# Kernel optimization log

Measured on AMD Instinct MI355X. Metric: run time of the kernel, lower is better.

## Reference

```python
import math
import jax, jax.numpy as jnp
import numpy as np

B, CK, H, W = 4, 64, 48, 84


def setup_inputs() -> dict:
    key = jax.random.key(0)
    k1, k2 = jax.random.split(key)
    mk = jax.random.normal(k1, (B, CK, 1, H, W), dtype=jnp.float32)
    qk = jax.random.normal(k2, (B, CK, H, W), dtype=jnp.float32)
    return {"mk": mk, "qk": qk}


def reference(mk, qk):
    b_, ck = mk.shape[0], mk.shape[1]
    mkf = mk.reshape(b_, ck, -1)            # [B, CK, N]  (N = T*H*W, T=1)
    qkf = qk.reshape(b_, ck, -1)            # [B, CK, M]  (M = H*W)
    a = jnp.sum(mkf * mkf, axis=1)[:, :, None]              # [B, N, 1]
    b = 2.0 * jnp.einsum('bcn,bcm->bnm', mkf, qkf)          # [B, N, M]
    c = jnp.sum(qkf * qkf, axis=1)[:, None, :]              # [B, 1, M]
    affinity = (-a + b - c) / math.sqrt(ck)                 # -||mk - qk||^2 / sqrt(CK)
    return jax.nn.softmax(affinity, axis=1)                 # softmax over memory axis
```

## Files before the change

kernel.cpp:

```cpp
#include <hip/hip_runtime.h>
#include <math.h>

#define B_  4
#define CK_ 64
#define N_  4032
#define M_  4032

#define P1_CHUNKS 7
#define P1_TILES  9
#define P2_GROUPS 9
#define P2_TILES  7

typedef __attribute__((ext_vector_type(8))) short short8;
typedef __attribute__((ext_vector_type(4))) float float4v;

__device__ inline unsigned short f2bf(float x) {
    unsigned u = __float_as_uint(x);
    u += 0x7FFF + ((u >> 16) & 1);
    return (unsigned short)(u >> 16);
}
__device__ inline float bf2f(unsigned short h) {
    return __uint_as_float(((unsigned)h) << 16);
}

__global__ __launch_bounds__(256) void prep_kernel(
    const float* __restrict__ mk, const float* __restrict__ qk,
    unsigned short* __restrict__ mk_hi, unsigned short* __restrict__ mk_lo,
    unsigned short* __restrict__ qk_hi, unsigned short* __restrict__ qk_lo,
    float* __restrict__ u)
{
    __shared__ float tile[64][65];
    __shared__ float sred[4][64];
    const int t  = threadIdx.x;
    const int n0 = blockIdx.x * 64;
    const int b  = blockIdx.y;
    const int which = blockIdx.z;

    const float* src = (which == 0 ? mk : qk) + (size_t)b * CK_ * N_;
    unsigned short* dhi = (which == 0 ? mk_hi : qk_hi) + (size_t)b * N_ * CK_;
    unsigned short* dlo = (which == 0 ? mk_lo : qk_lo) + (size_t)b * N_ * CK_;

    #pragma unroll
    for (int i = 0; i < 16; ++i) {
        const int idx = t + 256 * i;
        const int c = idx >> 6, n = idx & 63;
        tile[c][n] = src[(size_t)c * N_ + n0 + n];
    }
    __syncthreads();

    const int n = t & 63;
    const int g = t >> 6;
    unsigned short hbits[16], lbits[16];
    float ssq = 0.f;
    #pragma unroll
    for (int i = 0; i < 16; ++i) {
        const float x = tile[g * 16 + i][n];
        const unsigned short h = f2bf(x);
        hbits[i] = h;
        lbits[i] = f2bf(x - bf2f(h));
        ssq = fmaf(x, x, ssq);
    }
    {
        union { short8 v; unsigned short s[8]; } p0, p1, q0, q1;
        #pragma unroll
        for (int i = 0; i < 8; ++i) {
            p0.s[i] = hbits[i]; p1.s[i] = hbits[8 + i];
            q0.s[i] = lbits[i]; q1.s[i] = lbits[8 + i];
        }
        const size_t base = (size_t)(n0 + n) * CK_ + g * 16;
        *(short8*)(dhi + base)     = p0.v;
        *(short8*)(dhi + base + 8) = p1.v;
        *(short8*)(dlo + base)     = q0.v;
        *(short8*)(dlo + base + 8) = q1.v;
    }
    sred[g][n] = ssq;
    __syncthreads();
    if (which == 0 && t < 64) {
        const float tot = sred[0][t] + sred[1][t] + sred[2][t] + sred[3][t];
        u[(size_t)b * N_ + n0 + t] = __expf(-0.125f * tot);
    }
}


__global__ __launch_bounds__(256) void pass1_kernel(
    const unsigned short* __restrict__ mk_hi, const unsigned short* __restrict__ mk_lo,
    const unsigned short* __restrict__ qk_hi, const unsigned short* __restrict__ qk_lo,
    const float* __restrict__ u, float* __restrict__ psum)
{
    __shared__ float cs[2][64];
    const int t = threadIdx.x;
    const int wave = t >> 6, lane = t & 63;
    const int wn = wave & 1, wm = wave >> 1;
    const int lcol = lane & 15;
    const int quad = lane >> 4;
    const int chunk = blockIdx.y;
    const int b = blockIdx.z;
    const int m_base = blockIdx.x * 64 + wm * 32;

    const unsigned short* mh = mk_hi + (size_t)b * N_ * CK_;
    const unsigned short* ml = mk_lo + (size_t)b * N_ * CK_;
    const unsigned short* qh = qk_hi + (size_t)b * M_ * CK_;
    const unsigned short* ql = qk_lo + (size_t)b * M_ * CK_;
    const float* ub = u + (size_t)b * N_;

    short8 bh[2][2], bl[2][2];
    #pragma unroll
    for (int cg = 0; cg < 2; ++cg) {
        const size_t mrow = (size_t)(m_base + cg * 16 + lcol) * CK_;
        #pragma unroll
        for (int kc = 0; kc < 2; ++kc) {
            const size_t off = mrow + kc * 32 + quad * 8;
            bh[cg][kc] = *(const short8*)(qh + off);
            bl[cg][kc] = *(const short8*)(ql + off);
        }
    }

    float p0 = 0.f, p1 = 0.f;

    #pragma unroll 1
    for (int it = chunk * P1_TILES; it < chunk * P1_TILES + P1_TILES; ++it) {
        const int n_base = it * 64 + wn * 32;
        short8 ah[2][2], al[2][2];
        #pragma unroll
        for (int rg = 0; rg < 2; ++rg) {
            const size_t nrow = (size_t)(n_base + rg * 16 + lcol) * CK_;
            #pragma unroll
            for (int kc = 0; kc < 2; ++kc) {
                const size_t off = nrow + kc * 32 + quad * 8;
                ah[rg][kc] = *(const short8*)(mh + off);
                al[rg][kc] = *(const short8*)(ml + off);
            }
        }
        float uv[2][4];
        #pragma unroll
        for (int rg = 0; rg < 2; ++rg)
            #pragma unroll
            for (int r = 0; r < 4; ++r)
                uv[rg][r] = ub[n_base + rg * 16 + quad * 4 + r];

        #pragma unroll
        for (int rg = 0; rg < 2; ++rg) {
            #pragma unroll
            for (int cg = 0; cg < 2; ++cg) {
                float4v a1 = {0.f, 0.f, 0.f, 0.f};
                float4v a2 = {0.f, 0.f, 0.f, 0.f};
                #pragma unroll
                for (int kc = 0; kc < 2; ++kc) {
                    a1 = __builtin_amdgcn_mfma_f32_16x16x32_bf16(ah[rg][kc], bh[cg][kc], a1, 0, 0, 0);
                    a2 = __builtin_amdgcn_mfma_f32_16x16x32_bf16(ah[rg][kc], bl[cg][kc], a2, 0, 0, 0);
                    a2 = __builtin_amdgcn_mfma_f32_16x16x32_bf16(al[rg][kc], bh[cg][kc], a2, 0, 0, 0);
                }
                float ps = 0.f;
                #pragma unroll
                for (int r = 0; r < 4; ++r) {
                    const float dot = a1[r] + a2[r];
                    ps += uv[rg][r] * __expf(0.25f * dot);
                }
                if (cg == 0) p0 += ps; else p1 += ps;
            }
        }
    }

    p0 += __shfl_xor(p0, 16); p0 += __shfl_xor(p0, 32);
    p1 += __shfl_xor(p1, 16); p1 += __shfl_xor(p1, 32);
    if (lane < 16) {
        cs[wn][wm * 32 + lcol]      = p0;
        cs[wn][wm * 32 + 16 + lcol] = p1;
    }
    __syncthreads();
    if (t < 64) {
        psum[((size_t)b * P1_CHUNKS + chunk) * M_ + blockIdx.x * 64 + t] =
            cs[0][t] + cs[1][t];
    }
}

__global__ __launch_bounds__(256) void pass2_kernel(
    const unsigned short* __restrict__ mk_hi, const unsigned short* __restrict__ mk_lo,
    const unsigned short* __restrict__ qk_hi, const unsigned short* __restrict__ qk_lo,
    const float* __restrict__ u, const float* __restrict__ psum,
    float* __restrict__ out)
{
    const int t = threadIdx.x;
    const int wave = t >> 6, lane = t & 63;
    const int wn = wave & 1, wm = wave >> 1;
    const int lcol = lane & 15;
    const int quad = lane >> 4;
    const int b = blockIdx.z;
    const int m_base = blockIdx.x * 64 + wm * 32;

    const unsigned short* mh = mk_hi + (size_t)b * N_ * CK_;
    const unsigned short* ml = mk_lo + (size_t)b * N_ * CK_;
    const unsigned short* qh = qk_hi + (size_t)b * M_ * CK_;
    const unsigned short* ql = qk_lo + (size_t)b * M_ * CK_;
    const float* ub = u + (size_t)b * N_;

    short8 qah[2][2], qal[2][2];
    #pragma unroll
    for (int mg = 0; mg < 2; ++mg) {
        const size_t mrow = (size_t)(m_base + mg * 16 + lcol) * CK_;
        #pragma unroll
        for (int kc = 0; kc < 2; ++kc) {
            const size_t off = mrow + kc * 32 + quad * 8;
            qah[mg][kc] = *(const short8*)(qh + off);
            qal[mg][kc] = *(const short8*)(ql + off);
        }
    }

    float4v rinv4[2];
    #pragma unroll
    for (int mg = 0; mg < 2; ++mg) {
        float4v tot = {0.f, 0.f, 0.f, 0.f};
        #pragma unroll
        for (int c = 0; c < P1_CHUNKS; ++c) {
            const float4v p = *(const float4v*)(
                psum + ((size_t)b * P1_CHUNKS + c) * M_ + m_base + mg * 16 + quad * 4);
            tot += p;
        }
        rinv4[mg][0] = 1.f / tot[0];
        rinv4[mg][1] = 1.f / tot[1];
        rinv4[mg][2] = 1.f / tot[2];
        rinv4[mg][3] = 1.f / tot[3];
    }

    float* obase = out + (size_t)b * N_ * M_ + m_base + quad * 4;

    #pragma unroll 1
    for (int j = 0; j < P2_TILES; ++j) {
        const int n_base = (blockIdx.y * P2_TILES + j) * 64 + wn * 32;

        short8 bh[2][2], bl[2][2];
        #pragma unroll
        for (int ng = 0; ng < 2; ++ng) {
            const size_t nrow = (size_t)(n_base + ng * 16 + lcol) * CK_;
            #pragma unroll
            for (int kc = 0; kc < 2; ++kc) {
                const size_t off = nrow + kc * 32 + quad * 8;
                bh[ng][kc] = *(const short8*)(mh + off);
                bl[ng][kc] = *(const short8*)(ml + off);
            }
        }
        float un[2];
        #pragma unroll
        for (int ng = 0; ng < 2; ++ng)
            un[ng] = ub[n_base + ng * 16 + lcol];

        #pragma unroll
        for (int mg = 0; mg < 2; ++mg) {
            #pragma unroll
            for (int ng = 0; ng < 2; ++ng) {
                float4v a1 = {0.f, 0.f, 0.f, 0.f};
                float4v a2 = {0.f, 0.f, 0.f, 0.f};
                #pragma unroll
                for (int kc = 0; kc < 2; ++kc) {
                    a1 = __builtin_amdgcn_mfma_f32_16x16x32_bf16(qah[mg][kc], bh[ng][kc], a1, 0, 0, 0);
                    a2 = __builtin_amdgcn_mfma_f32_16x16x32_bf16(qah[mg][kc], bl[ng][kc], a2, 0, 0, 0);
                    a2 = __builtin_amdgcn_mfma_f32_16x16x32_bf16(qal[mg][kc], bh[ng][kc], a2, 0, 0, 0);
                }
                float4v v;
                #pragma unroll
                for (int r = 0; r < 4; ++r) {
                    const float dot = a1[r] + a2[r];
                    v[r] = un[ng] * __expf(0.25f * dot) * rinv4[mg][r];
                }
                float4v* dst = (float4v*)(
                    obase + (size_t)(n_base + ng * 16 + lcol) * M_ + mg * 16);
                __builtin_nontemporal_store(v, dst);
            }
        }
    }
}

extern "C" void kernel_launch(void* const* d_in, const int* in_sizes, int n_in,
                              void* d_out, int out_size, void* d_ws, size_t ws_size,
                              hipStream_t stream) {
    const float* mk = (const float*)d_in[0];
    const float* qk = (const float*)d_in[1];
    float* out = (float*)d_out;

    unsigned short* mk_hi = (unsigned short*)d_ws;
    unsigned short* mk_lo = mk_hi + (size_t)B_ * N_ * CK_;
    unsigned short* qk_hi = mk_lo + (size_t)B_ * N_ * CK_;
    unsigned short* qk_lo = qk_hi + (size_t)B_ * M_ * CK_;
    float* u    = (float*)(qk_lo + (size_t)B_ * M_ * CK_);
    float* psum = u + (size_t)B_ * N_;

    prep_kernel<<<dim3(N_ / 64, B_, 2), 256, 0, stream>>>(mk, qk, mk_hi, mk_lo, qk_hi, qk_lo, u);
    pass1_kernel<<<dim3(M_ / 64, P1_CHUNKS, B_), 256, 0, stream>>>(mk_hi, mk_lo, qk_hi, qk_lo, u, psum);
    pass2_kernel<<<dim3(M_ / 64, P2_GROUPS, B_), 256, 0, stream>>>(mk_hi, mk_lo, qk_hi, qk_lo, u, psum, out);
}
```

Before: 380.4 us.

## Pad N/M to 4096, use 512-thread blocks, unroll loops and raise MFMA priority

Pads the memory and query dimensions to 4096 with zeroed entries (u=0 for padded rows), so tile counts become powers of two. Blocks grow to 8 waves covering 128 query columns, main loops unroll by two, MFMA sections are wrapped in s_setprio, and the u values load as float4 vectors. The aim is better scheduling and latency hiding, with a guarded store that skips padded output. The cost is about 3% extra compute on padded rows plus a few branch checks.

```diff
diff --git a/kernel.cpp b/kernel.cpp
--- a/kernel.cpp
+++ b/kernel.cpp
@@ -5,11 +5,13 @@
 #define CK_ 64
 #define N_  4032
 #define M_  4032
-
-#define P1_CHUNKS 7
-#define P1_TILES  9
-#define P2_GROUPS 9
-#define P2_TILES  7
+#define NP_ 4096
+#define MP_ 4096
+
+#define P1C 8
+#define P1T 8
+#define P2G 8
+#define P2T 8
 
 typedef __attribute__((ext_vector_type(8))) short short8;
 typedef __attribute__((ext_vector_type(4))) float float4v;
@@ -35,16 +37,25 @@
     const int n0 = blockIdx.x * 64;
     const int b  = blockIdx.y;
     const int which = blockIdx.z;
+    const bool pad = (n0 >= N_);
 
     const float* src = (which == 0 ? mk : qk) + (size_t)b * CK_ * N_;
-    unsigned short* dhi = (which == 0 ? mk_hi : qk_hi) + (size_t)b * N_ * CK_;
-    unsigned short* dlo = (which == 0 ? mk_lo : qk_lo) + (size_t)b * N_ * CK_;
-
-    #pragma unroll
-    for (int i = 0; i < 16; ++i) {
-        const int idx = t + 256 * i;
-        const int c = idx >> 6, n = idx & 63;
-        tile[c][n] = src[(size_t)c * N_ + n0 + n];
+    unsigned short* dhi = (which == 0 ? mk_hi : qk_hi) + (size_t)b * NP_ * CK_;
+    unsigned short* dlo = (which == 0 ? mk_lo : qk_lo) + (size_t)b * NP_ * CK_;
+
+    if (!pad) {
+        #pragma unroll
+        for (int i = 0; i < 16; ++i) {
+            const int idx = t + 256 * i;
+            const int c = idx >> 6, n = idx & 63;
+            tile[c][n] = src[(size_t)c * N_ + n0 + n];
+        }
+    } else {
+        #pragma unroll
+        for (int i = 0; i < 16; ++i) {
+            const int idx = t + 256 * i;
+            tile[idx >> 6][idx & 63] = 0.f;
+        }
     }
     __syncthreads();
 
@@ -77,17 +88,17 @@
     __syncthreads();
     if (which == 0 && t < 64) {
         const float tot = sred[0][t] + sred[1][t] + sred[2][t] + sred[3][t];
-        u[(size_t)b * N_ + n0 + t] = __expf(-0.125f * tot);
-    }
-}
-
-
-__global__ __launch_bounds__(256) void pass1_kernel(
+        u[(size_t)b * NP_ + n0 + t] = pad ? 0.f : __expf(-0.125f * tot);
+    }
+}
+
+
+__global__ __launch_bounds__(512) void pass1_kernel(
     const unsigned short* __restrict__ mk_hi, const unsigned short* __restrict__ mk_lo,
     const unsigned short* __restrict__ qk_hi, const unsigned short* __restrict__ qk_lo,
     const float* __restrict__ u, float* __restrict__ psum)
 {
-    __shared__ float cs[2][64];
+    __shared__ float cs[2][128];
     const int t = threadIdx.x;
     const int wave = t >> 6, lane = t & 63;
     const int wn = wave & 1, wm = wave >> 1;
@@ -95,13 +106,13 @@
     const int quad = lane >> 4;
     const int chunk = blockIdx.y;
     const int b = blockIdx.z;
-    const int m_base = blockIdx.x * 64 + wm * 32;
-
-    const unsigned short* mh = mk_hi + (size_t)b * N_ * CK_;
-    const unsigned short* ml = mk_lo + (size_t)b * N_ * CK_;
-    const unsigned short* qh = qk_hi + (size_t)b * M_ * CK_;
-    const unsigned short* ql = qk_lo + (size_t)b * M_ * CK_;
-    const float* ub = u + (size_t)b * N_;
+    const int m_base = blockIdx.x * 128 + wm * 32;
+
+    const unsigned short* mh = mk_hi + (size_t)b * NP_ * CK_;
+    const unsigned short* ml = mk_lo + (size_t)b * NP_ * CK_;
+    const unsigned short* qh = qk_hi + (size_t)b * NP_ * CK_;
+    const unsigned short* ql = qk_lo + (size_t)b * NP_ * CK_;
+    const float* ub = u + (size_t)b * NP_;
 
     short8 bh[2][2], bl[2][2];
     #pragma unroll
@@ -117,8 +128,8 @@
 
     float p0 = 0.f, p1 = 0.f;
 
-    #pragma unroll 1
-    for (int it = chunk * P1_TILES; it < chunk * P1_TILES + P1_TILES; ++it) {
+    #pragma unroll 2
+    for (int it = chunk * P1T; it < chunk * P1T + P1T; ++it) {
         const int n_base = it * 64 + wn * 32;
         short8 ah[2][2], al[2][2];
         #pragma unroll
@@ -131,12 +142,8 @@
                 al[rg][kc] = *(const short8*)(ml + off);
             }
         }
-        float uv[2][4];
-        #pragma unroll
-        for (int rg = 0; rg < 2; ++rg)
-            #pragma unroll
-            for (int r = 0; r < 4; ++r)
-                uv[rg][r] = ub[n_base + rg * 16 + quad * 4 + r];
+        float4v uv0 = *(const float4v*)(ub + n_base + quad * 4);
+        float4v uv1 = *(const float4v*)(ub + n_base + 16 + quad * 4);
 
         #pragma unroll
         for (int rg = 0; rg < 2; ++rg) {
@@ -144,17 +151,20 @@
             for (int cg = 0; cg < 2; ++cg) {
                 float4v a1 = {0.f, 0.f, 0.f, 0.f};
                 float4v a2 = {0.f, 0.f, 0.f, 0.f};
+                __builtin_amdgcn_s_setprio(1);
                 #pragma unroll
                 for (int kc = 0; kc < 2; ++kc) {
                     a1 = __builtin_amdgcn_mfma_f32_16x16x32_bf16(ah[rg][kc], bh[cg][kc], a1, 0, 0, 0);
                     a2 = __builtin_amdgcn_mfma_f32_16x16x32_bf16(ah[rg][kc], bl[cg][kc], a2, 0, 0, 0);
                     a2 = __builtin_amdgcn_mfma_f32_16x16x32_bf16(al[rg][kc], bh[cg][kc], a2, 0, 0, 0);
                 }
+                __builtin_amdgcn_s_setprio(0);
                 float ps = 0.f;
                 #pragma unroll
                 for (int r = 0; r < 4; ++r) {
                     const float dot = a1[r] + a2[r];
-                    ps += uv[rg][r] * __expf(0.25f * dot);
+                    const float uvr = (rg == 0) ? uv0[r] : uv1[r];
+                    ps += uvr * __expf(0.25f * dot);
                 }
                 if (cg == 0) p0 += ps; else p1 += ps;
             }
@@ -168,13 +178,13 @@
         cs[wn][wm * 32 + 16 + lcol] = p1;
     }
     __syncthreads();
-    if (t < 64) {
-        psum[((size_t)b * P1_CHUNKS + chunk) * M_ + blockIdx.x * 64 + t] =
+    if (t < 128) {
+        psum[((size_t)b * P1C + chunk) * MP_ + blockIdx.x * 128 + t] =
             cs[0][t] + cs[1][t];
     }
 }
 
-__global__ __launch_bounds__(256) void pass2_kernel(
+__global__ __launch_bounds__(512) void pass2_kernel(
     const unsigned short* __restrict__ mk_hi, const unsigned short* __restrict__ mk_lo,
     const unsigned short* __restrict__ qk_hi, const unsigned short* __restrict__ qk_lo,
     const float* __restrict__ u, const float* __restrict__ psum,
@@ -186,13 +196,13 @@
     const int lcol = lane & 15;
     const int quad = lane >> 4;
     const int b = blockIdx.z;
-    const int m_base = blockIdx.x * 64 + wm * 32;
-
-    const unsigned short* mh = mk_hi + (size_t)b * N_ * CK_;
-    const unsigned short* ml = mk_lo + (size_t)b * N_ * CK_;
-    const unsigned short* qh = qk_hi + (size_t)b * M_ * CK_;
-    const unsigned short* ql = qk_lo + (size_t)b * M_ * CK_;
-    const float* ub = u + (size_t)b * N_;
+    const int m_base = blockIdx.x * 128 + wm * 32;
+
+    const unsigned short* mh = mk_hi + (size_t)b * NP_ * CK_;
+    const unsigned short* ml = mk_lo + (size_t)b * NP_ * CK_;
+    const unsigned short* qh = qk_hi + (size_t)b * NP_ * CK_;
+    const unsigned short* ql = qk_lo + (size_t)b * NP_ * CK_;
+    const float* ub = u + (size_t)b * NP_;
 
     short8 qah[2][2], qal[2][2];
     #pragma unroll
@@ -211,9 +221,9 @@
     for (int mg = 0; mg < 2; ++mg) {
         float4v tot = {0.f, 0.f, 0.f, 0.f};
         #pragma unroll
-        for (int c = 0; c < P1_CHUNKS; ++c) {
+        for (int c = 0; c < P1C; ++c) {
             const float4v p = *(const float4v*)(
-                psum + ((size_t)b * P1_CHUNKS + c) * M_ + m_base + mg * 16 + quad * 4);
+                psum + ((size_t)b * P1C + c) * MP_ + m_base + mg * 16 + quad * 4);
             tot += p;
         }
         rinv4[mg][0] = 1.f / tot[0];
@@ -222,11 +232,14 @@
         rinv4[mg][3] = 1.f / tot[3];
     }
 
+    const bool mval0 = (m_base < N_);
+    const bool mval1 = (m_base + 16 < N_);
+
     float* obase = out + (size_t)b * N_ * M_ + m_base + quad * 4;
 
-    #pragma unroll 1
-    for (int j = 0; j < P2_TILES; ++j) {
-        const int n_base = (blockIdx.y * P2_TILES + j) * 64 + wn * 32;
+    #pragma unroll 2
+    for (int j = 0; j < P2T; ++j) {
+        const int n_base = (blockIdx.y * P2T + j) * 64 + wn * 32;
 
         short8 bh[2][2], bl[2][2];
         #pragma unroll
@@ -244,27 +257,33 @@
         for (int ng = 0; ng < 2; ++ng)
             un[ng] = ub[n_base + ng * 16 + lcol];
 
+        const bool nval = (n_base < N_);
+
         #pragma unroll
         for (int mg = 0; mg < 2; ++mg) {
             #pragma unroll
             for (int ng = 0; ng < 2; ++ng) {
                 float4v a1 = {0.f, 0.f, 0.f, 0.f};
                 float4v a2 = {0.f, 0.f, 0.f, 0.f};
+                __builtin_amdgcn_s_setprio(1);
                 #pragma unroll
                 for (int kc = 0; kc < 2; ++kc) {
                     a1 = __builtin_amdgcn_mfma_f32_16x16x32_bf16(qah[mg][kc], bh[ng][kc], a1, 0, 0, 0);
                     a2 = __builtin_amdgcn_mfma_f32_16x16x32_bf16(qah[mg][kc], bl[ng][kc], a2, 0, 0, 0);
                     a2 = __builtin_amdgcn_mfma_f32_16x16x32_bf16(qal[mg][kc], bh[ng][kc], a2, 0, 0, 0);
                 }
+                __builtin_amdgcn_s_setprio(0);
                 float4v v;
                 #pragma unroll
                 for (int r = 0; r < 4; ++r) {
                     const float dot = a1[r] + a2[r];
                     v[r] = un[ng] * __expf(0.25f * dot) * rinv4[mg][r];
                 }
-                float4v* dst = (float4v*)(
-                    obase + (size_t)(n_base + ng * 16 + lcol) * M_ + mg * 16);
-                __builtin_nontemporal_store(v, dst);
+                if (nval && (mg == 0 ? mval0 : mval1)) {
+                    float4v* dst = (float4v*)(
+                        obase + (size_t)(n_base + ng * 16 + lcol) * M_ + mg * 16);
+                    __builtin_nontemporal_store(v, dst);
+                }
             }
         }
     }
@@ -278,13 +297,13 @@
     float* out = (float*)d_out;
 
     unsigned short* mk_hi = (unsigned short*)d_ws;
-    unsigned short* mk_lo = mk_hi + (size_t)B_ * N_ * CK_;
-    unsigned short* qk_hi = mk_lo + (size_t)B_ * N_ * CK_;
-    unsigned short* qk_lo = qk_hi + (size_t)B_ * M_ * CK_;
-    float* u    = (float*)(qk_lo + (size_t)B_ * M_ * CK_);
-    float* psum = u + (size_t)B_ * N_;
-
-    prep_kernel<<<dim3(N_ / 64, B_, 2), 256, 0, stream>>>(mk, qk, mk_hi, mk_lo, qk_hi, qk_lo, u);
-    pass1_kernel<<<dim3(M_ / 64, P1_CHUNKS, B_), 256, 0, stream>>>(mk_hi, mk_lo, qk_hi, qk_lo, u, psum);
-    pass2_kernel<<<dim3(M_ / 64, P2_GROUPS, B_), 256, 0, stream>>>(mk_hi, mk_lo, qk_hi, qk_lo, u, psum, out);
-}
+    unsigned short* mk_lo = mk_hi + (size_t)B_ * NP_ * CK_;
+    unsigned short* qk_hi = mk_lo + (size_t)B_ * NP_ * CK_;
+    unsigned short* qk_lo = qk_hi + (size_t)B_ * NP_ * CK_;
+    float* u    = (float*)(qk_lo + (size_t)B_ * NP_ * CK_);
+    float* psum = u + (size_t)B_ * NP_;
+
+    prep_kernel<<<dim3(NP_ / 64, B_, 2), 256, 0, stream>>>(mk, qk, mk_hi, mk_lo, qk_hi, qk_lo, u);
+    pass1_kernel<<<dim3(MP_ / 128, P1C, B_), 512, 0, stream>>>(mk_hi, mk_lo, qk_hi, qk_lo, u, psum);
+    pass2_kernel<<<dim3(MP_ / 128, P2G, B_), 512, 0, stream>>>(mk_hi, mk_lo, qk_hi, qk_lo, u, psum, out);
+}
```

New measurement: 377.2 us. Within noise of the previous version (-0.8%).
